# Kernel tuning notes

Measured on AMD Instinct MI355X. Metric: run time of the kernel, lower is better.

## Reference

```python
import jax, jax.numpy as jnp
import numpy as np

B, C, Cs, CI, H, W = 4, 256, 256, 128, 64, 64

def setup_inputs() -> dict:
    key = jax.random.key(0)
    ks = jax.random.split(key, 9)
    sq = 1.0 / np.sqrt(C)
    ss = 1.0 / np.sqrt(Cs)
    return {
        "x_main": jax.random.normal(ks[0], (B, C, H, W), jnp.float32),
        "z_p": jax.random.normal(ks[1], (B, Cs, H, W), jnp.float32),
        "Wq": jax.random.normal(ks[2], (CI, C), jnp.float32) * sq,
        "bq": jax.random.normal(ks[3], (CI,), jnp.float32) * 0.01,
        "Wk": jax.random.normal(ks[4], (CI, Cs), jnp.float32) * ss,
        "bk": jax.random.normal(ks[5], (CI,), jnp.float32) * 0.01,
        "Wv": jax.random.normal(ks[6], (C, Cs), jnp.float32) * ss,
        "bv": jax.random.normal(ks[7], (C,), jnp.float32) * 0.01,
        "gamma": jax.random.normal(ks[8], (1,), jnp.float32) * 0.1,
    }

def reference(x_main, z_p, Wq, bq, Wk, bk, Wv, bv, gamma):
    b, c, h, w = x_main.shape
    n = h * w
    xm = x_main.reshape(b, c, n)          # [B, C, N]
    zf = z_p.reshape(b, z_p.shape[1], n)  # [B, Cs, M] (M == N here)
    # 1x1 convs == per-pixel channel projections
    q = jnp.einsum('oc,bcn->bon', Wq, xm) + bq[None, :, None]  # [B, CI, N]
    k = jnp.einsum('oc,bcm->bom', Wk, zf) + bk[None, :, None]  # [B, CI, M]
    v = jnp.einsum('oc,bcm->bom', Wv, zf) + bv[None, :, None]  # [B, C, M]
    # energy[b, n, m] = q_n . k_m  (no scaling, as in the original)
    energy = jnp.einsum('bcn,bcm->bnm', q, k)
    attention = jax.nn.softmax(energy, axis=-1)
    out = jnp.einsum('bom,bnm->bon', v, attention)  # [B, C, N]
    out = out.reshape(b, c, h, w)
    return gamma * out + x_main
```

## Files before the change

kernel.cpp:

```cpp
#include <hip/hip_runtime.h>
#include <hip/hip_bf16.h>


typedef __bf16  bf16x8  __attribute__((ext_vector_type(8)));
typedef float   f32x16  __attribute__((ext_vector_type(16)));

#define LOG2E 1.4426950408889634f

union BF8 { __hip_bfloat162 h[4]; bf16x8 v; };
union U4  { unsigned u[4]; bf16x8 v; };

__device__ inline bf16x8 pack8(const float f[8]) {
  BF8 u;
#pragma unroll
  for (int i = 0; i < 4; i++)
    u.h[i] = __float22bfloat162_rn(float2{f[2 * i], f[2 * i + 1]});
  return u.v;
}

__device__ inline void dma16(const void* g, void* l) {
  __builtin_amdgcn_global_load_lds(
      (const __attribute__((address_space(1))) unsigned int*)g,
      (__attribute__((address_space(3))) unsigned int*)l, 16, 0, 0);
}

__global__ __launch_bounds__(256) void prep_kernel(
    const float* __restrict__ x, const float* __restrict__ z,
    const float* __restrict__ Wq, const float* __restrict__ Wk,
    const float* __restrict__ Wv,
    __hip_bfloat16* __restrict__ xf, __hip_bfloat16* __restrict__ zf,
    __hip_bfloat16* __restrict__ wfr)
{
  __shared__ float lds[256 * 68];
  const int bi = blockIdx.x;
  const int tid = threadIdx.x;
  if (bi < 512) {
    const int sel = bi >> 8;
    const int b   = (bi >> 6) & 3;
    const int pc  = bi & 63;
    const float* in = sel ? z : x;
    __hip_bfloat16* outp = sel ? zf : xf;
    const size_t ib = (size_t)b * 256 * 4096 + pc * 64;
    const int pix4 = (tid & 15) * 4;
#pragma unroll
    for (int it = 0; it < 16; it++) {
      int ch = it * 16 + (tid >> 4);
      float4 v4 = *(const float4*)&in[ib + (size_t)ch * 4096 + pix4];
      *(float4*)&lds[ch * 68 + pix4] = v4;
    }
    __syncthreads();
    const size_t ob = ((size_t)(b * 128 + pc * 2)) * 8192;
#pragma unroll
    for (int i = 0; i < 8; i++) {
      int c = i * 256 + tid;
      int grp = c >> 10, cs = (c >> 6) & 15, rem = c & 63;
      int hf = rem >> 5, l32 = rem & 31;
      float f[8];
      int chb = cs * 16 + hf * 8;
#pragma unroll
      for (int j = 0; j < 8; j++)
        f[j] = lds[(chb + j) * 68 + grp * 32 + l32];
      *(bf16x8*)(outp + ob + grp * 8192 + cs * 512 + hf * 256 + l32 * 8) =
          pack8(f);
    }
  } else {
    const int base = (bi - 512) * 4096;
#pragma unroll
    for (int i = 0; i < 16; i++) {
      int c = base + i * 256 + tid;
      const float* Ws; __hip_bfloat16* dst; int rc;
      if (c < 4096)      { Ws = Wq; dst = wfr;          rc = c; }
      else if (c < 8192) { Ws = Wk; dst = wfr + 32768;  rc = c - 4096; }
      else               { Ws = Wv; dst = wfr + 65536;  rc = c - 8192; }
      int ot = rc >> 10, cs = (rc >> 6) & 15, rem = rc & 63;
      int hf = rem >> 5, l32 = rem & 31;
      const float* src = Ws + (ot * 32 + l32) * 256 + cs * 16 + hf * 8;
      float f[8];
#pragma unroll
      for (int j = 0; j < 8; j++) f[j] = src[j];
      *(bf16x8*)(dst + ot * 8192 + cs * 512 + hf * 256 + l32 * 8) = pack8(f);
    }
  }
}

__global__ __launch_bounds__(256, 3) void proj_mfma(
    const __hip_bfloat16* __restrict__ xf, const __hip_bfloat16* __restrict__ zf,
    const __hip_bfloat16* __restrict__ wfr,
    const float* __restrict__ bq, const float* __restrict__ bk,
    const float* __restrict__ bv,
    __hip_bfloat16* __restrict__ qp, __hip_bfloat16* __restrict__ kp,
    __hip_bfloat16* __restrict__ vp)
{
  const int bi = blockIdx.x;
  int mode, b, pg0, h = 0;
  if (bi < 512) { mode = bi >> 8; b = (bi >> 6) & 3; pg0 = (bi & 63) * 2; }
  else { int j = bi - 512; mode = 2; b = j >> 7; pg0 = ((j >> 1) & 63) * 2; h = j & 1; }
  const int tid = threadIdx.x, w = tid >> 6, lane = tid & 63,
            l32 = lane & 31, half = lane >> 5;

  const __hip_bfloat16* X = (mode == 0) ? xf : zf;
  const int wtile = (mode == 2 ? h * 4 : 0) + w;
  const int wbase = (mode == 0) ? 0 : (mode == 1) ? 32768 : 65536;
  const __hip_bfloat16* wp = wfr + wbase + wtile * 8192 + lane * 8;
  bf16x8 wfg[16];
#pragma unroll
  for (int cs = 0; cs < 16; cs++) wfg[cs] = *(const bf16x8*)(wp + cs * 512);

  const float* bias = (mode == 0) ? bq : (mode == 1) ? bk : bv;
  const int ochb = (mode == 2 ? h * 128 : 0) + w * 32;
  float bb[16];
#pragma unroll
  for (int r = 0; r < 16; r++)
    bb[r] = bias[ochb + (r & 3) + 8 * (r >> 2) + 4 * half];

  const int t4 = (l32 >> 2) & 3;
  const int kperm = (t4 == 1 || t4 == 2) ? (l32 ^ 12) : l32;

  const __hip_bfloat16* xb0 = X + ((size_t)(b * 128 + pg0)) * 8192 + lane * 8;
  const __hip_bfloat16* xb1 = xb0 + 8192;
  f32x16 O0 = {}, O1 = {};
#pragma unroll
  for (int cs = 0; cs < 16; cs++) {
    bf16x8 xr0 = *(const bf16x8*)(xb0 + cs * 512);
    bf16x8 xr1 = *(const bf16x8*)(xb1 + cs * 512);
    O0 = __builtin_amdgcn_mfma_f32_32x32x16_bf16(wfg[cs], xr0, O0, 0, 0, 0);
    O1 = __builtin_amdgcn_mfma_f32_32x32x16_bf16(wfg[cs], xr1, O1, 0, 0, 0);
  }
#pragma unroll
  for (int p = 0; p < 2; p++) {
    const f32x16& O = p ? O1 : O0;
    const int pg = pg0 + p;
    if (mode == 0) {
      __hip_bfloat16* qb = qp + ((size_t)(b * 128 + pg)) * 4096;
#pragma unroll
      for (int r = 0; r < 16; r++) {
        int oc = ochb + (r & 3) + 8 * (r >> 2) + 4 * half;
        qb[(oc >> 4) * 512 + ((oc >> 3) & 1) * 256 + l32 * 8 + (oc & 7)] =
            __float2bfloat16((O[r] + bb[r]) * LOG2E);
      }
    } else if (mode == 1) {
      __hip_bfloat16* kb = kp + ((size_t)(b * 128 + pg)) * 4096;
#pragma unroll
      for (int r = 0; r < 16; r++) {
        int oc = ochb + (r & 3) + 8 * (r >> 2) + 4 * half;
        kb[(oc >> 4) * 512 + ((oc >> 3) & 1) * 256 + kperm * 8 + (oc & 7)] =
            __float2bfloat16(O[r] + bb[r]);
      }
    } else {
      __hip_bfloat16* vb = vp + ((size_t)(b * 128 + pg)) * 8192
          + (h * 4 + w) * 1024 + (l32 >> 4) * 512 + ((l32 >> 3) & 1) * 256
          + (l32 & 7);
#pragma unroll
      for (int r = 0; r < 16; r++) {
        int rr = (r & 3) + 8 * (r >> 2) + 4 * half;
        vb[rr * 8] = __float2bfloat16(O[r] + bb[r]);
      }
    }
  }
}

struct AttnSmem {
  union {
    __hip_bfloat16 kbuf[3][8192];
    float ostage[256][33];
  } u;
  float redu[4][32];
  float rinv[32];
};

__global__ __launch_bounds__(256, 3) void attn_kernel(
    const __hip_bfloat16* __restrict__ qv, const __hip_bfloat16* __restrict__ kv,
    const __hip_bfloat16* __restrict__ vv,
    const float* __restrict__ x_main, const float* __restrict__ gammap,
    float* __restrict__ out)
{
  __shared__ AttnSmem sm;
  const int i  = blockIdx.x;
  const int b  = (i & 7) >> 1;
  const int qt = ((i >> 3) << 1) | (i & 1);
  const int n0 = qt * 32;
  const int tid  = threadIdx.x;
  const int w    = tid >> 6, lane = tid & 63, l32 = lane & 31;
  const int kh   = w >> 1, chh = w & 1;
  const int t0   = qt & 63;

  bf16x8 qf[8];
  {
    const __hip_bfloat16* qb = qv + ((size_t)(b * 128 + qt)) * 4096 + lane * 8;
#pragma unroll
    for (int cs = 0; cs < 8; cs++) qf[cs] = *(const bf16x8*)(qb + cs * 512);
  }

  const __hip_bfloat16* kg = kv + (size_t)(b * 128) * 4096;
  const __hip_bfloat16* vg = vv + (size_t)(b * 128) * 8192;

  auto stage = [&](int ta, int par) {
    __hip_bfloat16* kd = sm.u.kbuf[par];
    const __hip_bfloat16* ksrc = kg + (size_t)ta * 8192 + lane * 8;
#pragma unroll
    for (int c = 0; c < 4; c++) {
      int ck = w * 4 + c;
      dma16(ksrc + ck * 512, kd + ck * 512 + lane * 8);
    }
  };

  f32x16 Oacc[4];
#pragma unroll
  for (int c = 0; c < 4; c++)
#pragma unroll
    for (int r = 0; r < 16; r++) Oacc[c][r] = 0.f;

  float l_lane = 0.f;

  stage(t0, 0);
  stage((t0 + 1) & 63, 1);
  __syncthreads();

#pragma unroll 1
  for (int lt = 0; lt < 64; ++lt) {
    const int ta = (lt + t0) & 63;

    const __hip_bfloat16* vb = vg + (size_t)(ta * 2 + kh) * 8192
                             + chh * 4096 + lane * 8;
    bf16x8 Vc[8];
#pragma unroll
    for (int c = 0; c < 4; c++) {
      Vc[2 * c]     = *(const bf16x8*)(vb + c * 1024);
      Vc[2 * c + 1] = *(const bf16x8*)(vb + c * 1024 + 512);
    }
    __builtin_amdgcn_sched_barrier(0);

    if (lt < 62) stage((lt + 2 + t0) & 63, (lt + 2) % 3);

    const __hip_bfloat16* kbase = sm.u.kbuf[lt % 3] + kh * 4096 + lane * 8;
    f32x16 S = {};
#pragma unroll
    for (int cs = 0; cs < 8; cs++) {
      bf16x8 kf = *(const bf16x8*)(kbase + cs * 512);
      S = __builtin_amdgcn_mfma_f32_32x32x16_bf16(kf, qf[cs], S, 0, 0, 0);
    }

    unsigned p2[8];
    float lsub = 0.f;
#pragma unroll
    for (int i2 = 0; i2 < 8; i2++) {
      float a = exp2f(S[2 * i2]     - 64.0f);
      float c = exp2f(S[2 * i2 + 1] - 64.0f);
      lsub += a + c;
      union { __hip_bfloat162 h; unsigned u; } cv;
      cv.h = __float22bfloat162_rn(float2{a, c});
      p2[i2] = cv.u;
    }
    l_lane += lsub;
    U4 f0, f1;
    f0.u[0] = p2[0]; f0.u[1] = p2[1]; f0.u[2] = p2[2]; f0.u[3] = p2[3];
    f1.u[0] = p2[4]; f1.u[1] = p2[5]; f1.u[2] = p2[6]; f1.u[3] = p2[7];
    const bf16x8 pf0 = f0.v, pf1 = f1.v;

#pragma unroll
    for (int c = 0; c < 4; c++) {
      Oacc[c] = __builtin_amdgcn_mfma_f32_32x32x16_bf16(Vc[2 * c],     pf0, Oacc[c], 0, 0, 0);
      Oacc[c] = __builtin_amdgcn_mfma_f32_32x32x16_bf16(Vc[2 * c + 1], pf1, Oacc[c], 0, 0, 0);
    }

    if (lt < 63) {
      __builtin_amdgcn_sched_barrier(0);
      __builtin_amdgcn_s_barrier();
      __builtin_amdgcn_sched_barrier(0);
    }
  }

  float lfull = l_lane + __shfl_xor(l_lane, 32);
  if (lane < 32) sm.redu[w][l32] = lfull;
  __syncthreads();
  const int hb = lane >> 5;
  if (kh == 0) {
#pragma unroll
    for (int c = 0; c < 4; c++) {
#pragma unroll
      for (int r = 0; r < 16; r++) {
        int ch = (chh * 4 + c) * 32 + (r & 3) + 8 * (r >> 2) + 4 * hb;
        sm.u.ostage[ch][l32] = Oacc[c][r];
      }
    }
  }
  if (tid < 32) sm.rinv[tid] = 1.0f / (sm.redu[0][tid] + sm.redu[2][tid]);
  __syncthreads();
  if (kh == 1) {
#pragma unroll
    for (int c = 0; c < 4; c++) {
#pragma unroll
      for (int r = 0; r < 16; r++) {
        int ch = (chh * 4 + c) * 32 + (r & 3) + 8 * (r >> 2) + 4 * hb;
        sm.u.ostage[ch][l32] += Oacc[c][r];
      }
    }
  }
  __syncthreads();

  const float gmm = gammap[0];
  const int pix = tid & 31;
  const float ri = sm.rinv[pix];
#pragma unroll
  for (int j = 0; j < 32; ++j) {
    int ch = (tid >> 5) * 32 + j;
    size_t g = ((size_t)(b * 256 + ch)) * 4096 + n0 + pix;
    out[g] = gmm * sm.u.ostage[ch][pix] * ri + x_main[g];
  }
}

extern "C" void kernel_launch(void* const* d_in, const int* in_sizes, int n_in,
                              void* d_out, int out_size, void* d_ws, size_t ws_size,
                              hipStream_t stream) {
  (void)in_sizes; (void)n_in; (void)out_size; (void)ws_size;
  const float* x  = (const float*)d_in[0];
  const float* z  = (const float*)d_in[1];
  const float* Wq = (const float*)d_in[2];
  const float* bq = (const float*)d_in[3];
  const float* Wk = (const float*)d_in[4];
  const float* bk = (const float*)d_in[5];
  const float* Wv = (const float*)d_in[6];
  const float* bv = (const float*)d_in[7];
  const float* gm = (const float*)d_in[8];
  float* out = (float*)d_out;

  char* ws = (char*)d_ws;
  const size_t MB = 1024 * 1024;
  __hip_bfloat16* qp  = (__hip_bfloat16*)(ws);
  __hip_bfloat16* kp  = (__hip_bfloat16*)(ws + 4 * MB);
  __hip_bfloat16* vp  = (__hip_bfloat16*)(ws + 8 * MB);
  __hip_bfloat16* xfp = (__hip_bfloat16*)(ws + 16 * MB);
  __hip_bfloat16* zfp = (__hip_bfloat16*)(ws + 24 * MB);
  __hip_bfloat16* wfp = (__hip_bfloat16*)(ws + 32 * MB);

  prep_kernel<<<516, 256, 0, stream>>>(x, z, Wq, Wk, Wv, xfp, zfp, wfp);
  proj_mfma  <<<1024, 256, 0, stream>>>(xfp, zfp, wfp, bq, bk, bv, qp, kp, vp);
  attn_kernel<<<512, 256, 0, stream>>>(qp, kp, vp, x, gm, out);
}
```

Baseline: 212.2 us.

## Split key tiles across waves with direct global loads and LDS atomic reduction

The attention kernel now gives each wave its own key tile per iteration and has it cover all 256 output channels, instead of splitting keys in halves and channels in halves across waves. K is loaded straight from global memory into registers rather than triple-buffered into LDS with DMA, which removes the per-iteration block barrier. Partial outputs from the four waves are summed in LDS with atomic adds. This doubles the accumulator registers per wave (occupancy hint lowered from 3 to 2 blocks) and adds an s_setprio around the PV MFMAs. It trades LDS staging and barrier cost for more register pressure and more global traffic per wave.

```diff
diff --git a/kernel.cpp b/kernel.cpp
--- a/kernel.cpp
+++ b/kernel.cpp
@@ -16,12 +16,6 @@
   for (int i = 0; i < 4; i++)
     u.h[i] = __float22bfloat162_rn(float2{f[2 * i], f[2 * i + 1]});
   return u.v;
-}
-
-__device__ inline void dma16(const void* g, void* l) {
-  __builtin_amdgcn_global_load_lds(
-      (const __attribute__((address_space(1))) unsigned int*)g,
-      (__attribute__((address_space(3))) unsigned int*)l, 16, 0, 0);
 }
 
 __global__ __launch_bounds__(256) void prep_kernel(
@@ -160,15 +154,12 @@
 }
 
 struct AttnSmem {
-  union {
-    __hip_bfloat16 kbuf[3][8192];
-    float ostage[256][33];
-  } u;
+  float ost[256][33];
   float redu[4][32];
   float rinv[32];
 };
 
-__global__ __launch_bounds__(256, 3) void attn_kernel(
+__global__ __launch_bounds__(256, 2) void attn_kernel(
     const __hip_bfloat16* __restrict__ qv, const __hip_bfloat16* __restrict__ kv,
     const __hip_bfloat16* __restrict__ vv,
     const float* __restrict__ x_main, const float* __restrict__ gammap,
@@ -180,9 +171,8 @@
   const int qt = ((i >> 3) << 1) | (i & 1);
   const int n0 = qt * 32;
   const int tid  = threadIdx.x;
-  const int w    = tid >> 6, lane = tid & 63, l32 = lane & 31;
-  const int kh   = w >> 1, chh = w & 1;
-  const int t0   = qt & 63;
+  const int w    = tid >> 6, lane = tid & 63, l32 = lane & 31, hb = lane >> 5;
+  const int t0   = qt & 31;
 
   bf16x8 qf[8];
   {
@@ -194,50 +184,34 @@
   const __hip_bfloat16* kg = kv + (size_t)(b * 128) * 4096;
   const __hip_bfloat16* vg = vv + (size_t)(b * 128) * 8192;
 
-  auto stage = [&](int ta, int par) {
-    __hip_bfloat16* kd = sm.u.kbuf[par];
-    const __hip_bfloat16* ksrc = kg + (size_t)ta * 8192 + lane * 8;
-#pragma unroll
-    for (int c = 0; c < 4; c++) {
-      int ck = w * 4 + c;
-      dma16(ksrc + ck * 512, kd + ck * 512 + lane * 8);
-    }
-  };
-
-  f32x16 Oacc[4];
-#pragma unroll
-  for (int c = 0; c < 4; c++)
-#pragma unroll
-    for (int r = 0; r < 16; r++) Oacc[c][r] = 0.f;
+  f32x16 Oacc[8];
+#pragma unroll
+  for (int cg = 0; cg < 8; cg++)
+#pragma unroll
+    for (int r = 0; r < 16; r++) Oacc[cg][r] = 0.f;
 
   float l_lane = 0.f;
 
-  stage(t0, 0);
-  stage((t0 + 1) & 63, 1);
-  __syncthreads();
-
 #pragma unroll 1
-  for (int lt = 0; lt < 64; ++lt) {
-    const int ta = (lt + t0) & 63;
-
-    const __hip_bfloat16* vb = vg + (size_t)(ta * 2 + kh) * 8192
-                             + chh * 4096 + lane * 8;
-    bf16x8 Vc[8];
-#pragma unroll
-    for (int c = 0; c < 4; c++) {
-      Vc[2 * c]     = *(const bf16x8*)(vb + c * 1024);
-      Vc[2 * c + 1] = *(const bf16x8*)(vb + c * 1024 + 512);
-    }
-    __builtin_amdgcn_sched_barrier(0);
-
-    if (lt < 62) stage((lt + 2 + t0) & 63, (lt + 2) % 3);
-
-    const __hip_bfloat16* kbase = sm.u.kbuf[lt % 3] + kh * 4096 + lane * 8;
+  for (int lt = 0; lt < 32; ++lt) {
+    const int g4 = ((lt + t0) & 31) * 4 + w;
+    const __hip_bfloat16* kb = kg + (size_t)g4 * 4096 + lane * 8;
+    const __hip_bfloat16* vb = vg + (size_t)g4 * 8192 + lane * 8;
+
+    bf16x8 kf[8];
+#pragma unroll
+    for (int cs = 0; cs < 8; cs++) kf[cs] = *(const bf16x8*)(kb + cs * 512);
+
     f32x16 S = {};
 #pragma unroll
-    for (int cs = 0; cs < 8; cs++) {
-      bf16x8 kf = *(const bf16x8*)(kbase + cs * 512);
-      S = __builtin_amdgcn_mfma_f32_32x32x16_bf16(kf, qf[cs], S, 0, 0, 0);
+    for (int cs = 0; cs < 8; cs++)
+      S = __builtin_amdgcn_mfma_f32_32x32x16_bf16(kf[cs], qf[cs], S, 0, 0, 0);
+
+    bf16x8 Va[8];
+#pragma unroll
+    for (int cg = 0; cg < 4; cg++) {
+      Va[2 * cg]     = *(const bf16x8*)(vb + cg * 1024);
+      Va[2 * cg + 1] = *(const bf16x8*)(vb + cg * 1024 + 512);
     }
 
     unsigned p2[8];
@@ -257,45 +231,53 @@
     f1.u[0] = p2[4]; f1.u[1] = p2[5]; f1.u[2] = p2[6]; f1.u[3] = p2[7];
     const bf16x8 pf0 = f0.v, pf1 = f1.v;
 
-#pragma unroll
-    for (int c = 0; c < 4; c++) {
-      Oacc[c] = __builtin_amdgcn_mfma_f32_32x32x16_bf16(Vc[2 * c],     pf0, Oacc[c], 0, 0, 0);
-      Oacc[c] = __builtin_amdgcn_mfma_f32_32x32x16_bf16(Vc[2 * c + 1], pf1, Oacc[c], 0, 0, 0);
-    }
-
-    if (lt < 63) {
-      __builtin_amdgcn_sched_barrier(0);
-      __builtin_amdgcn_s_barrier();
-      __builtin_amdgcn_sched_barrier(0);
-    }
+    bf16x8 Vb2[8];
+#pragma unroll
+    for (int cg = 0; cg < 4; cg++) {
+      Vb2[2 * cg]     = *(const bf16x8*)(vb + 4096 + cg * 1024);
+      Vb2[2 * cg + 1] = *(const bf16x8*)(vb + 4096 + cg * 1024 + 512);
+    }
+
+    __builtin_amdgcn_s_setprio(1);
+#pragma unroll
+    for (int cg = 0; cg < 4; cg++) {
+      Oacc[cg] = __builtin_amdgcn_mfma_f32_32x32x16_bf16(Va[2 * cg],     pf0, Oacc[cg], 0, 0, 0);
+      Oacc[cg] = __builtin_amdgcn_mfma_f32_32x32x16_bf16(Va[2 * cg + 1], pf1, Oacc[cg], 0, 0, 0);
+    }
+#pragma unroll
+    for (int cg = 0; cg < 4; cg++) {
+      Oacc[4 + cg] = __builtin_amdgcn_mfma_f32_32x32x16_bf16(Vb2[2 * cg],     pf0, Oacc[4 + cg], 0, 0, 0);
+      Oacc[4 + cg] = __builtin_amdgcn_mfma_f32_32x32x16_bf16(Vb2[2 * cg + 1], pf1, Oacc[4 + cg], 0, 0, 0);
+    }
+    __builtin_amdgcn_s_setprio(0);
   }
 
   float lfull = l_lane + __shfl_xor(l_lane, 32);
   if (lane < 32) sm.redu[w][l32] = lfull;
+  if (w == 0) {
+#pragma unroll
+    for (int cg = 0; cg < 8; cg++) {
+#pragma unroll
+      for (int r = 0; r < 16; r++) {
+        int ch = cg * 32 + (r & 3) + 8 * (r >> 2) + 4 * hb;
+        sm.ost[ch][l32] = Oacc[cg][r];
+      }
+    }
+  }
   __syncthreads();
-  const int hb = lane >> 5;
-  if (kh == 0) {
-#pragma unroll
-    for (int c = 0; c < 4; c++) {
-#pragma unroll
-      for (int r = 0; r < 16; r++) {
-        int ch = (chh * 4 + c) * 32 + (r & 3) + 8 * (r >> 2) + 4 * hb;
-        sm.u.ostage[ch][l32] = Oacc[c][r];
-      }
-    }
-  }
-  if (tid < 32) sm.rinv[tid] = 1.0f / (sm.redu[0][tid] + sm.redu[2][tid]);
-  __syncthreads();
-  if (kh == 1) {
-#pragma unroll
-    for (int c = 0; c < 4; c++) {
-#pragma unroll
-      for (int r = 0; r < 16; r++) {
-        int ch = (chh * 4 + c) * 32 + (r & 3) + 8 * (r >> 2) + 4 * hb;
-        sm.u.ostage[ch][l32] += Oacc[c][r];
-      }
-    }
-  }
+  if (w != 0) {
+#pragma unroll
+    for (int cg = 0; cg < 8; cg++) {
+#pragma unroll
+      for (int r = 0; r < 16; r++) {
+        int ch = cg * 32 + (r & 3) + 8 * (r >> 2) + 4 * hb;
+        atomicAdd(&sm.ost[ch][l32], Oacc[cg][r]);
+      }
+    }
+  }
+  if (tid < 32)
+    sm.rinv[tid] = 1.0f / (sm.redu[0][tid] + sm.redu[1][tid] +
+                           sm.redu[2][tid] + sm.redu[3][tid]);
   __syncthreads();
 
   const float gmm = gammap[0];
@@ -305,7 +287,7 @@
   for (int j = 0; j < 32; ++j) {
     int ch = (tid >> 5) * 32 + j;
     size_t g = ((size_t)(b * 256 + ch)) * 4096 + n0 + pix;
-    out[g] = gmm * sm.u.ostage[ch][pix] * ri + x_main[g];
+    out[g] = gmm * sm.ost[ch][pix] * ri + x_main[g];
   }
 }
 
```

Result: slower. 239.1 us (+12.7%).

## Fuse activation bf16 conversion into projection kernel via LDS staging

Applied to the files above, without the earlier changes.

Splits weight preparation into its own small kernel and fuses the x/z fp32-to-bf16 fragment conversion directly into the projection kernel. Each 512-thread block stages 64 pixels × 256 channels through LDS in two halves, builds MFMA fragments in shared memory, and then computes Q, or K and V together, from the shared fragments. This removes the intermediate bf16 xf/zf global round trip and reuses the z fragments for both K and V. The cost is larger LDS use per block, more serialized syncs, and lower occupancy.

```diff
diff --git a/kernel.cpp b/kernel.cpp
--- a/kernel.cpp
+++ b/kernel.cpp
@@ -24,136 +24,165 @@
       (__attribute__((address_space(3))) unsigned int*)l, 16, 0, 0);
 }
 
-__global__ __launch_bounds__(256) void prep_kernel(
+__global__ __launch_bounds__(256) void wprep_kernel(
+    const float* __restrict__ Wq, const float* __restrict__ Wk,
+    const float* __restrict__ Wv, __hip_bfloat16* __restrict__ wfr)
+{
+  const int base = blockIdx.x * 1024;
+  const int tid = threadIdx.x;
+#pragma unroll
+  for (int i = 0; i < 4; i++) {
+    int c = base + i * 256 + tid;
+    const float* Ws; __hip_bfloat16* dst; int rc;
+    if (c < 4096)      { Ws = Wq; dst = wfr;          rc = c; }
+    else if (c < 8192) { Ws = Wk; dst = wfr + 32768;  rc = c - 4096; }
+    else               { Ws = Wv; dst = wfr + 65536;  rc = c - 8192; }
+    int ot = rc >> 10, cs = (rc >> 6) & 15, rem = rc & 63;
+    int hf = rem >> 5, l32 = rem & 31;
+    const float* src = Ws + (ot * 32 + l32) * 256 + cs * 16 + hf * 8;
+    float f[8];
+#pragma unroll
+    for (int j = 0; j < 8; j++) f[j] = src[j];
+    *(bf16x8*)(dst + ot * 8192 + cs * 512 + hf * 256 + l32 * 8) = pack8(f);
+  }
+}
+
+struct PFSmem {
+  float stg[128 * 68];
+  alignas(16) __hip_bfloat16 frag[16384];
+};
+
+__global__ __launch_bounds__(512, 2) void projfused(
     const float* __restrict__ x, const float* __restrict__ z,
-    const float* __restrict__ Wq, const float* __restrict__ Wk,
-    const float* __restrict__ Wv,
-    __hip_bfloat16* __restrict__ xf, __hip_bfloat16* __restrict__ zf,
-    __hip_bfloat16* __restrict__ wfr)
-{
-  __shared__ float lds[256 * 68];
-  const int bi = blockIdx.x;
-  const int tid = threadIdx.x;
-  if (bi < 512) {
-    const int sel = bi >> 8;
-    const int b   = (bi >> 6) & 3;
-    const int pc  = bi & 63;
-    const float* in = sel ? z : x;
-    __hip_bfloat16* outp = sel ? zf : xf;
-    const size_t ib = (size_t)b * 256 * 4096 + pc * 64;
-    const int pix4 = (tid & 15) * 4;
-#pragma unroll
-    for (int it = 0; it < 16; it++) {
-      int ch = it * 16 + (tid >> 4);
-      float4 v4 = *(const float4*)&in[ib + (size_t)ch * 4096 + pix4];
-      *(float4*)&lds[ch * 68 + pix4] = v4;
-    }
-    __syncthreads();
-    const size_t ob = ((size_t)(b * 128 + pc * 2)) * 8192;
-#pragma unroll
-    for (int i = 0; i < 8; i++) {
-      int c = i * 256 + tid;
-      int grp = c >> 10, cs = (c >> 6) & 15, rem = c & 63;
-      int hf = rem >> 5, l32 = rem & 31;
-      float f[8];
-      int chb = cs * 16 + hf * 8;
-#pragma unroll
-      for (int j = 0; j < 8; j++)
-        f[j] = lds[(chb + j) * 68 + grp * 32 + l32];
-      *(bf16x8*)(outp + ob + grp * 8192 + cs * 512 + hf * 256 + l32 * 8) =
-          pack8(f);
-    }
-  } else {
-    const int base = (bi - 512) * 4096;
-#pragma unroll
-    for (int i = 0; i < 16; i++) {
-      int c = base + i * 256 + tid;
-      const float* Ws; __hip_bfloat16* dst; int rc;
-      if (c < 4096)      { Ws = Wq; dst = wfr;          rc = c; }
-      else if (c < 8192) { Ws = Wk; dst = wfr + 32768;  rc = c - 4096; }
-      else               { Ws = Wv; dst = wfr + 65536;  rc = c - 8192; }
-      int ot = rc >> 10, cs = (rc >> 6) & 15, rem = rc & 63;
-      int hf = rem >> 5, l32 = rem & 31;
-      const float* src = Ws + (ot * 32 + l32) * 256 + cs * 16 + hf * 8;
-      float f[8];
-#pragma unroll
-      for (int j = 0; j < 8; j++) f[j] = src[j];
-      *(bf16x8*)(dst + ot * 8192 + cs * 512 + hf * 256 + l32 * 8) = pack8(f);
-    }
-  }
-}
-
-__global__ __launch_bounds__(256, 3) void proj_mfma(
-    const __hip_bfloat16* __restrict__ xf, const __hip_bfloat16* __restrict__ zf,
     const __hip_bfloat16* __restrict__ wfr,
     const float* __restrict__ bq, const float* __restrict__ bk,
     const float* __restrict__ bv,
     __hip_bfloat16* __restrict__ qp, __hip_bfloat16* __restrict__ kp,
     __hip_bfloat16* __restrict__ vp)
 {
+  __shared__ PFSmem sm;
   const int bi = blockIdx.x;
-  int mode, b, pg0, h = 0;
-  if (bi < 512) { mode = bi >> 8; b = (bi >> 6) & 3; pg0 = (bi & 63) * 2; }
-  else { int j = bi - 512; mode = 2; b = j >> 7; pg0 = ((j >> 1) & 63) * 2; h = j & 1; }
+  const bool qmode = bi < 256;
+  const int j2 = qmode ? bi : bi - 256;
+  const int b = j2 >> 6, pc = j2 & 63;
+  const float* in = qmode ? x : z;
+  const size_t ib = (size_t)b * 256 * 4096 + pc * 64;
+
   const int tid = threadIdx.x, w = tid >> 6, lane = tid & 63,
             l32 = lane & 31, half = lane >> 5;
-
-  const __hip_bfloat16* X = (mode == 0) ? xf : zf;
-  const int wtile = (mode == 2 ? h * 4 : 0) + w;
-  const int wbase = (mode == 0) ? 0 : (mode == 1) ? 32768 : 65536;
-  const __hip_bfloat16* wp = wfr + wbase + wtile * 8192 + lane * 8;
-  bf16x8 wfg[16];
-#pragma unroll
-  for (int cs = 0; cs < 16; cs++) wfg[cs] = *(const bf16x8*)(wp + cs * 512);
-
-  const float* bias = (mode == 0) ? bq : (mode == 1) ? bk : bv;
-  const int ochb = (mode == 2 ? h * 128 : 0) + w * 32;
-  float bb[16];
-#pragma unroll
-  for (int r = 0; r < 16; r++)
-    bb[r] = bias[ochb + (r & 3) + 8 * (r >> 2) + 4 * half];
+  const int pix4 = (tid & 15) * 4;
+
+#pragma unroll
+  for (int it = 0; it < 4; it++) {
+    int ch = it * 32 + (tid >> 4);
+    float4 v4 = *(const float4*)&in[ib + (size_t)ch * 4096 + pix4];
+    *(float4*)&sm.stg[ch * 68 + pix4] = v4;
+  }
+  __syncthreads();
+#pragma unroll
+  for (int i = 0; i < 2; i++) {
+    int c = i * 512 + tid;
+    int grp = c >> 9, csl = (c >> 6) & 7, rem = c & 63;
+    int hf = rem >> 5, lr = rem & 31;
+    int chb = csl * 16 + hf * 8;
+    float f[8];
+#pragma unroll
+    for (int j = 0; j < 8; j++) f[j] = sm.stg[(chb + j) * 68 + grp * 32 + lr];
+    *(bf16x8*)(sm.frag + grp * 8192 + csl * 512 + hf * 256 + lr * 8) = pack8(f);
+  }
+  __syncthreads();
+
+#pragma unroll
+  for (int it = 0; it < 4; it++) {
+    int ch = it * 32 + (tid >> 4);
+    float4 v4 = *(const float4*)&in[ib + (size_t)(128 + ch) * 4096 + pix4];
+    *(float4*)&sm.stg[ch * 68 + pix4] = v4;
+  }
+  __syncthreads();
+#pragma unroll
+  for (int i = 0; i < 2; i++) {
+    int c = i * 512 + tid;
+    int grp = c >> 9, csl = (c >> 6) & 7, rem = c & 63;
+    int hf = rem >> 5, lr = rem & 31;
+    int chb = csl * 16 + hf * 8;
+    float f[8];
+#pragma unroll
+    for (int j = 0; j < 8; j++) f[j] = sm.stg[(chb + j) * 68 + grp * 32 + lr];
+    *(bf16x8*)(sm.frag + grp * 8192 + (csl + 8) * 512 + hf * 256 + lr * 8) =
+        pack8(f);
+  }
+  __syncthreads();
 
   const int t4 = (l32 >> 2) & 3;
   const int kperm = (t4 == 1 || t4 == 2) ? (l32 ^ 12) : l32;
 
-  const __hip_bfloat16* xb0 = X + ((size_t)(b * 128 + pg0)) * 8192 + lane * 8;
-  const __hip_bfloat16* xb1 = xb0 + 8192;
-  f32x16 O0 = {}, O1 = {};
-#pragma unroll
-  for (int cs = 0; cs < 16; cs++) {
-    bf16x8 xr0 = *(const bf16x8*)(xb0 + cs * 512);
-    bf16x8 xr1 = *(const bf16x8*)(xb1 + cs * 512);
-    O0 = __builtin_amdgcn_mfma_f32_32x32x16_bf16(wfg[cs], xr0, O0, 0, 0, 0);
-    O1 = __builtin_amdgcn_mfma_f32_32x32x16_bf16(wfg[cs], xr1, O1, 0, 0, 0);
-  }
-#pragma unroll
-  for (int p = 0; p < 2; p++) {
-    const f32x16& O = p ? O1 : O0;
-    const int pg = pg0 + p;
-    if (mode == 0) {
-      __hip_bfloat16* qb = qp + ((size_t)(b * 128 + pg)) * 4096;
-#pragma unroll
-      for (int r = 0; r < 16; r++) {
-        int oc = ochb + (r & 3) + 8 * (r >> 2) + 4 * half;
-        qb[(oc >> 4) * 512 + ((oc >> 3) & 1) * 256 + l32 * 8 + (oc & 7)] =
-            __float2bfloat16((O[r] + bb[r]) * LOG2E);
-      }
-    } else if (mode == 1) {
-      __hip_bfloat16* kb = kp + ((size_t)(b * 128 + pg)) * 4096;
-#pragma unroll
-      for (int r = 0; r < 16; r++) {
-        int oc = ochb + (r & 3) + 8 * (r >> 2) + 4 * half;
-        kb[(oc >> 4) * 512 + ((oc >> 3) & 1) * 256 + kperm * 8 + (oc & 7)] =
-            __float2bfloat16(O[r] + bb[r]);
-      }
-    } else {
-      __hip_bfloat16* vb = vp + ((size_t)(b * 128 + pg)) * 8192
-          + (h * 4 + w) * 1024 + (l32 >> 4) * 512 + ((l32 >> 3) & 1) * 256
-          + (l32 & 7);
-#pragma unroll
-      for (int r = 0; r < 16; r++) {
-        int rr = (r & 3) + 8 * (r >> 2) + 4 * half;
-        vb[rr * 8] = __float2bfloat16(O[r] + bb[r]);
+  if (qmode) {
+    const int ot = w >> 1, pg = w & 1;
+    bf16x8 bfr[16];
+#pragma unroll
+    for (int cs = 0; cs < 16; cs++)
+      bfr[cs] = *(const bf16x8*)(sm.frag + pg * 8192 + cs * 512 + lane * 8);
+    const __hip_bfloat16* wp = wfr + ot * 8192 + lane * 8;
+    bf16x8 wfg[16];
+#pragma unroll
+    for (int cs = 0; cs < 16; cs++) wfg[cs] = *(const bf16x8*)(wp + cs * 512);
+    float bb[16];
+#pragma unroll
+    for (int r = 0; r < 16; r++)
+      bb[r] = bq[ot * 32 + (r & 3) + 8 * (r >> 2) + 4 * half];
+    f32x16 O = {};
+#pragma unroll
+    for (int cs = 0; cs < 16; cs++)
+      O = __builtin_amdgcn_mfma_f32_32x32x16_bf16(wfg[cs], bfr[cs], O, 0, 0, 0);
+    __hip_bfloat16* qb = qp + ((size_t)(b * 128 + pc * 2 + pg)) * 4096;
+#pragma unroll
+    for (int r = 0; r < 16; r++) {
+      int oc = ot * 32 + (r & 3) + 8 * (r >> 2) + 4 * half;
+      qb[(oc >> 4) * 512 + ((oc >> 3) & 1) * 256 + l32 * 8 + (oc & 7)] =
+          __float2bfloat16((O[r] + bb[r]) * LOG2E);
+    }
+  } else {
+    const int pg = w & 1;
+    bf16x8 bfr[16];
+#pragma unroll
+    for (int cs = 0; cs < 16; cs++)
+      bfr[cs] = *(const bf16x8*)(sm.frag + pg * 8192 + cs * 512 + lane * 8);
+    const size_t pgg = (size_t)(b * 128 + pc * 2 + pg);
+#pragma unroll
+    for (int jj = 0; jj < 3; jj++) {
+      const int t = (w + jj * 8) >> 1;
+      const bool isK = (t < 4);
+      const __hip_bfloat16* wp = wfr + (isK ? 32768 + t * 8192
+                                            : 65536 + (t - 4) * 8192) + lane * 8;
+      bf16x8 wfg[16];
+#pragma unroll
+      for (int cs = 0; cs < 16; cs++) wfg[cs] = *(const bf16x8*)(wp + cs * 512);
+      const float* bias = isK ? bk : bv;
+      const int ocb = (isK ? t : t - 4) * 32;
+      float bb[16];
+#pragma unroll
+      for (int r = 0; r < 16; r++)
+        bb[r] = bias[ocb + (r & 3) + 8 * (r >> 2) + 4 * half];
+      f32x16 O = {};
+#pragma unroll
+      for (int cs = 0; cs < 16; cs++)
+        O = __builtin_amdgcn_mfma_f32_32x32x16_bf16(wfg[cs], bfr[cs], O, 0, 0, 0);
+      if (isK) {
+        __hip_bfloat16* kb = kp + pgg * 4096;
+#pragma unroll
+        for (int r = 0; r < 16; r++) {
+          int oc = t * 32 + (r & 3) + 8 * (r >> 2) + 4 * half;
+          kb[(oc >> 4) * 512 + ((oc >> 3) & 1) * 256 + kperm * 8 + (oc & 7)] =
+              __float2bfloat16(O[r] + bb[r]);
+        }
+      } else {
+        __hip_bfloat16* vb = vp + pgg * 8192 + (t - 4) * 1024
+            + (l32 >> 4) * 512 + ((l32 >> 3) & 1) * 256 + (l32 & 7);
+#pragma unroll
+        for (int r = 0; r < 16; r++) {
+          int rr = (r & 3) + 8 * (r >> 2) + 4 * half;
+          vb[rr * 8] = __float2bfloat16(O[r] + bb[r]);
+        }
       }
     }
   }
@@ -329,11 +358,9 @@
   __hip_bfloat16* qp  = (__hip_bfloat16*)(ws);
   __hip_bfloat16* kp  = (__hip_bfloat16*)(ws + 4 * MB);
   __hip_bfloat16* vp  = (__hip_bfloat16*)(ws + 8 * MB);
-  __hip_bfloat16* xfp = (__hip_bfloat16*)(ws + 16 * MB);
-  __hip_bfloat16* zfp = (__hip_bfloat16*)(ws + 24 * MB);
-  __hip_bfloat16* wfp = (__hip_bfloat16*)(ws + 32 * MB);
-
-  prep_kernel<<<516, 256, 0, stream>>>(x, z, Wq, Wk, Wv, xfp, zfp, wfp);
-  proj_mfma  <<<1024, 256, 0, stream>>>(xfp, zfp, wfp, bq, bk, bv, qp, kp, vp);
-  attn_kernel<<<512, 256, 0, stream>>>(qp, kp, vp, x, gm, out);
-}
+  __hip_bfloat16* wfp = (__hip_bfloat16*)(ws + 16 * MB);
+
+  wprep_kernel<<<16, 256, 0, stream>>>(Wq, Wk, Wv, wfp);
+  projfused   <<<512, 512, 0, stream>>>(x, z, wfp, bq, bk, bv, qp, kp, vp);
+  attn_kernel <<<512, 256, 0, stream>>>(qp, kp, vp, x, gm, out);
+}
```

After: 202.6 us. 1.05x faster.
